# Kernel tuning notes

Measured on AMD Instinct MI355X. Metric: run time of the kernel, lower is better.

## Reference

```python
import jax, jax.numpy as jnp
import numpy as np


def setup_inputs() -> dict:
    key = jax.random.key(0)
    k1, k2, k3, k4 = jax.random.split(key, 4)
    B, N, D_in, H, P = 16, 4096, 588, 1152, 4096
    pixel_values = jax.random.uniform(k1, (B, N, D_in), dtype=jnp.float32)
    pixel_position_ids = jax.random.randint(k2, (B, N, 2), 0, P, dtype=jnp.int64)
    padding_positions = jnp.zeros((B, N), dtype=bool)
    W_proj = jax.random.normal(k3, (D_in, H), dtype=jnp.float32) * (D_in ** -0.5)
    pos_table = jax.random.normal(k4, (2, P, H), dtype=jnp.float32)
    return {
        "pixel_values": pixel_values,
        "pixel_position_ids": pixel_position_ids,
        "padding_positions": padding_positions,
        "W_proj": W_proj,
        "pos_table": pos_table,
    }


def reference(pixel_values, pixel_position_ids, padding_positions, W_proj, pos_table):
    # Patch projection: patches = 2*(x - 0.5); Linear(no bias).
    patches = 2.0 * (pixel_values - 0.5)
    hidden = jnp.einsum("bnd,dh->bnh", patches, W_proj)  # [B,N,H]

    # Position embeddings: one_hot @ table summed over the 2 (row/col) axis
    # == gather of table rows. Same math, no [B,2,N,P] intermediate.
    pos = jnp.maximum(pixel_position_ids, 0)  # clamp(min=0), [B,N,2]
    pe = pos_table[0][pos[..., 0]] + pos_table[1][pos[..., 1]]  # [B,N,H]
    pe = jnp.where(padding_positions[..., None], 0.0, pe)

    return hidden + pe
```

## Files before the change

kernel.cpp:

```cpp
#include <hip/hip_runtime.h>
#include <hip/hip_bf16.h>
#include <stdint.h>

#define M_TOTAL   65536
#define K_ORIG    588
#define K_PAD     608
#define H_DIM     1152
#define P_DIM     4096
#define KT_STEPS  19

typedef short bf16x8 __attribute__((ext_vector_type(8)));
typedef float f32x4  __attribute__((ext_vector_type(4)));

__device__ __forceinline__ unsigned short f2bf(float f) {
  __hip_bfloat16 h = __float2bfloat16(f);
  return __builtin_bit_cast(unsigned short, h);
}

__device__ __forceinline__ void gload_lds16(const void* g, void* s) {
  __builtin_amdgcn_global_load_lds(
      (const __attribute__((address_space(1))) void*)g,
      (__attribute__((address_space(3))) void*)s, 16, 0, 0);
}

__global__ void convert_patches(const float* __restrict__ px,
                                unsigned short* __restrict__ out) {
  const int64_t i = (int64_t)blockIdx.x * blockDim.x + threadIdx.x;
  const int g = (int)(i % 152);
  const int64_t m = i / 152;
  const int k0 = g * 4;
  ushort4 o;
  if (k0 < K_ORIG) {
    const float4 v = *(const float4*)(px + m * K_ORIG + k0);
    o.x = f2bf(2.f * v.x - 1.f);
    o.y = f2bf(2.f * v.y - 1.f);
    o.z = f2bf(2.f * v.z - 1.f);
    o.w = f2bf(2.f * v.w - 1.f);
  } else {
    o.x = 0; o.y = 0; o.z = 0; o.w = 0;
  }
  *(ushort4*)(out + m * K_PAD + k0) = o;
}

__global__ void convert_w(const float* __restrict__ W,
                          unsigned short* __restrict__ Wt) {
  const int i = blockIdx.x * blockDim.x + threadIdx.x;
  const int k = i % K_PAD;
  const int h = i / K_PAD;
  Wt[i] = (k < K_ORIG) ? f2bf(W[(int64_t)k * H_DIM + h]) : (unsigned short)0;
}

__global__ void __launch_bounds__(256) gemm_fused(
    const unsigned short* __restrict__ A,
    const unsigned short* __restrict__ Bt,
    const int* __restrict__ ids,
    const unsigned char* __restrict__ padm,
    const float* __restrict__ ptab,
    float* __restrict__ out) {
  __shared__ __align__(16) unsigned short Ash[128 * 32];
  __shared__ __align__(16) unsigned short Bsh[128 * 32];
  __shared__ int p0s[128];
  __shared__ int p1s[128];
  __shared__ unsigned char mks[128];

  const int tid = threadIdx.x;
  const int w   = tid >> 6;
  const int l   = tid & 63;
  const int bm  = blockIdx.x / 9;
  const int bn  = blockIdx.x % 9;
  const int wm  = w >> 1;
  const int wn  = w & 1;

  if (tid < 128) {
    const int gm = bm * 128 + tid;
    const int q0 = ids[2 * gm + 0];
    const int q1 = ids[2 * gm + 1];
    p0s[tid] = q0 < 0 ? 0 : q0;
    p1s[tid] = q1 < 0 ? 0 : q1;
    mks[tid] = padm[gm];
  }

  f32x4 acc[4][4];
#pragma unroll
  for (int i = 0; i < 4; ++i)
#pragma unroll
    for (int j = 0; j < 4; ++j) acc[i][j] = f32x4{0.f, 0.f, 0.f, 0.f};

  const int srow = l >> 2;
  const int sk   = ((l & 3) ^ ((l >> 3) & 3)) * 8;
  const int64_t abase = (int64_t)(bm * 128) * K_PAD;
  const int64_t bbase = (int64_t)(bn * 128) * K_PAD;

  int ra[4], rb[4];
#pragma unroll
  for (int mi = 0; mi < 4; ++mi) {
    const int rA = wm * 64 + mi * 16 + (l & 15);
    ra[mi] = rA * 32 + (((l >> 4) ^ ((rA >> 1) & 3)) * 8);
    const int rB = wn * 64 + mi * 16 + (l & 15);
    rb[mi] = rB * 32 + (((l >> 4) ^ ((rB >> 1) & 3)) * 8);
  }

  for (int kt = 0; kt < KT_STEPS; ++kt) {
    const int k0 = kt * 32;
#pragma unroll
    for (int i = 0; i < 2; ++i) {
      const int r0 = (w * 2 + i) * 16;
      gload_lds16(A + abase + (int64_t)(r0 + srow) * K_PAD + k0 + sk,
                  &Ash[r0 * 32]);
      gload_lds16(Bt + bbase + (int64_t)(r0 + srow) * K_PAD + k0 + sk,
                  &Bsh[r0 * 32]);
    }
    __syncthreads();

    bf16x8 av[4], bv[4];
#pragma unroll
    for (int mi = 0; mi < 4; ++mi) av[mi] = *(const bf16x8*)&Ash[ra[mi]];
#pragma unroll
    for (int ni = 0; ni < 4; ++ni) bv[ni] = *(const bf16x8*)&Bsh[rb[ni]];
#pragma unroll
    for (int mi = 0; mi < 4; ++mi)
#pragma unroll
      for (int ni = 0; ni < 4; ++ni)
        acc[mi][ni] = __builtin_amdgcn_mfma_f32_16x16x32_bf16(
            av[mi], bv[ni], acc[mi][ni], 0, 0, 0);
    __syncthreads();
  }

  const int c  = l & 15;
  const int rg = (l >> 4) * 4;
  const float* T0 = ptab;
  const float* T1 = ptab + (int64_t)P_DIM * H_DIM;
  const int hcol0 = bn * 128 + wn * 64;

#pragma unroll
  for (int mi = 0; mi < 4; ++mi) {
#pragma unroll
    for (int j = 0; j < 4; ++j) {
      const int r = wm * 64 + mi * 16 + rg + j;
      const int64_t gm = (int64_t)bm * 128 + r;
      const bool pad = mks[r] != 0;
      const float* t0 = T0 + (int64_t)p0s[r] * H_DIM;
      const float* t1 = T1 + (int64_t)p1s[r] * H_DIM;
      float* orow = out + gm * H_DIM;
#pragma unroll
      for (int ni = 0; ni < 4; ++ni) {
        const int gh = hcol0 + ni * 16 + c;
        const float pe = pad ? 0.f : (t0[gh] + t1[gh]);
        orow[gh] = acc[mi][ni][j] + pe;
      }
    }
  }
}

extern "C" void kernel_launch(void* const* d_in, const int* in_sizes, int n_in,
                              void* d_out, int out_size, void* d_ws,
                              size_t ws_size, hipStream_t stream) {
  const float* px            = (const float*)d_in[0];
  const int* ids             = (const int*)d_in[1];
  const unsigned char* padm  = (const unsigned char*)d_in[2];
  const float* W             = (const float*)d_in[3];
  const float* pt            = (const float*)d_in[4];
  float* out                 = (float*)d_out;

  unsigned short* Apad = (unsigned short*)d_ws;
  unsigned short* Wt   = Apad + (size_t)M_TOTAL * K_PAD;

  convert_patches<<<38912, 256, 0, stream>>>(px, Apad);
  convert_w<<<2736, 256, 0, stream>>>(W, Wt);
  gemm_fused<<<4608, 256, 0, stream>>>(Apad, Wt, ids, padm, pt, out);
}
```

Baseline: 651.9 us.

## Fuse patch fp32-to-bf16 conversion into GEMM with double-buffered LDS pipeline

Drops the separate convert_patches pass. The GEMM now reads fp32 pixel values directly into registers, scales and converts them to bf16, and writes them into swizzled LDS. A double-buffered LDS scheme prefetches the next K-tile of A (through registers) and B (direct-to-LDS) while the current tile is computed, which halves the number of barriers. It also remaps block indices so that consecutive blocks spread across groups, and rewrites the weight transpose to use a shared-memory tile for coalesced access. The cost is that each of the 9 column blocks per row tile re-reads and re-converts the fp32 A tile, at twice the bytes of bf16, and register and LDS use go up.

```diff
diff --git a/kernel.cpp b/kernel.cpp
--- a/kernel.cpp
+++ b/kernel.cpp
@@ -23,42 +23,36 @@
       (__attribute__((address_space(3))) void*)s, 16, 0, 0);
 }
 
-__global__ void convert_patches(const float* __restrict__ px,
-                                unsigned short* __restrict__ out) {
-  const int64_t i = (int64_t)blockIdx.x * blockDim.x + threadIdx.x;
-  const int g = (int)(i % 152);
-  const int64_t m = i / 152;
-  const int k0 = g * 4;
-  ushort4 o;
-  if (k0 < K_ORIG) {
-    const float4 v = *(const float4*)(px + m * K_ORIG + k0);
-    o.x = f2bf(2.f * v.x - 1.f);
-    o.y = f2bf(2.f * v.y - 1.f);
-    o.z = f2bf(2.f * v.z - 1.f);
-    o.w = f2bf(2.f * v.w - 1.f);
-  } else {
-    o.x = 0; o.y = 0; o.z = 0; o.w = 0;
-  }
-  *(ushort4*)(out + m * K_PAD + k0) = o;
-}
-
-__global__ void convert_w(const float* __restrict__ W,
-                          unsigned short* __restrict__ Wt) {
-  const int i = blockIdx.x * blockDim.x + threadIdx.x;
-  const int k = i % K_PAD;
-  const int h = i / K_PAD;
-  Wt[i] = (k < K_ORIG) ? f2bf(W[(int64_t)k * H_DIM + h]) : (unsigned short)0;
+__global__ void __launch_bounds__(256) convert_w(const float* __restrict__ W,
+                                                 unsigned short* __restrict__ Wt) {
+  __shared__ float tile[32][33];
+  const int kt = blockIdx.x % 19;
+  const int ht = blockIdx.x / 19;
+  const int k0 = kt * 32, h0 = ht * 32;
+  const int r = threadIdx.x >> 5;
+  const int c = threadIdx.x & 31;
+#pragma unroll
+  for (int i = 0; i < 4; ++i) {
+    const int k = k0 + r + i * 8;
+    tile[r + i * 8][c] = (k < K_ORIG) ? W[(int64_t)k * H_DIM + h0 + c] : 0.f;
+  }
+  __syncthreads();
+#pragma unroll
+  for (int i = 0; i < 4; ++i) {
+    const int h = h0 + r + i * 8;
+    Wt[(int64_t)h * K_PAD + k0 + c] = f2bf(tile[c][r + i * 8]);
+  }
 }
 
 __global__ void __launch_bounds__(256) gemm_fused(
-    const unsigned short* __restrict__ A,
+    const float* __restrict__ px,
     const unsigned short* __restrict__ Bt,
     const int* __restrict__ ids,
     const unsigned char* __restrict__ padm,
     const float* __restrict__ ptab,
     float* __restrict__ out) {
-  __shared__ __align__(16) unsigned short Ash[128 * 32];
-  __shared__ __align__(16) unsigned short Bsh[128 * 32];
+  __shared__ __align__(16) unsigned short Ash[2][128 * 32];
+  __shared__ __align__(16) unsigned short Bsh[2][128 * 32];
   __shared__ int p0s[128];
   __shared__ int p1s[128];
   __shared__ unsigned char mks[128];
@@ -66,8 +60,11 @@
   const int tid = threadIdx.x;
   const int w   = tid >> 6;
   const int l   = tid & 63;
-  const int bm  = blockIdx.x / 9;
-  const int bn  = blockIdx.x % 9;
+
+  const int bid = blockIdx.x;
+  const int lin = (bid >> 3) + (bid & 7) * 576;
+  const int bm  = lin / 9;
+  const int bn  = lin % 9;
   const int wm  = w >> 1;
   const int wn  = w & 1;
 
@@ -88,8 +85,12 @@
 
   const int srow = l >> 2;
   const int sk   = ((l & 3) ^ ((l >> 3) & 3)) * 8;
-  const int64_t abase = (int64_t)(bm * 128) * K_PAD;
   const int64_t bbase = (int64_t)(bn * 128) * K_PAD;
+
+  const int arow = tid >> 3;
+  const int achk = tid & 7;
+  const int64_t arowbase = (int64_t)(bm * 128) * K_ORIG;
+  f32x4 areg[4];
 
   int ra[4], rb[4];
 #pragma unroll
@@ -100,30 +101,73 @@
     rb[mi] = rB * 32 + (((l >> 4) ^ ((rB >> 1) & 3)) * 8);
   }
 
-  for (int kt = 0; kt < KT_STEPS; ++kt) {
+  auto stageB = [&](int kt, int buf) {
     const int k0 = kt * 32;
 #pragma unroll
     for (int i = 0; i < 2; ++i) {
       const int r0 = (w * 2 + i) * 16;
-      gload_lds16(A + abase + (int64_t)(r0 + srow) * K_PAD + k0 + sk,
-                  &Ash[r0 * 32]);
       gload_lds16(Bt + bbase + (int64_t)(r0 + srow) * K_PAD + k0 + sk,
-                  &Bsh[r0 * 32]);
-    }
-    __syncthreads();
+                  &Bsh[buf][r0 * 32]);
+    }
+  };
+
+  auto loadA = [&](int kt) {
+    const int k = kt * 32 + achk * 4;
+    const bool v = (k < K_ORIG);
+    const f32x4 zero = {0.f, 0.f, 0.f, 0.f};
+#pragma unroll
+    for (int rb4 = 0; rb4 < 4; ++rb4) {
+      const int row = rb4 * 32 + arow;
+      areg[rb4] = v ? *(const f32x4*)(px + arowbase + (int64_t)row * K_ORIG + k)
+                    : zero;
+    }
+  };
+
+  auto writeA = [&](int buf) {
+    const int g   = achk >> 1;
+    const int sub = (achk & 1) * 4;
+#pragma unroll
+    for (int rb4 = 0; rb4 < 4; ++rb4) {
+      const int row = rb4 * 32 + arow;
+      const int off = row * 32 + ((g ^ ((row >> 1) & 3)) * 8) + sub;
+      ushort4 o;
+      o.x = f2bf(__builtin_fmaf(2.f, areg[rb4][0], -1.f));
+      o.y = f2bf(__builtin_fmaf(2.f, areg[rb4][1], -1.f));
+      o.z = f2bf(__builtin_fmaf(2.f, areg[rb4][2], -1.f));
+      o.w = f2bf(__builtin_fmaf(2.f, areg[rb4][3], -1.f));
+      *(ushort4*)&Ash[buf][off] = o;
+    }
+  };
+
+  loadA(0);
+  stageB(0, 0);
+  writeA(0);
+  __syncthreads();
+
+  for (int t = 0; t < KT_STEPS; ++t) {
+    const int cur = t & 1;
+    const bool more = (t + 1 < KT_STEPS);
+    if (more) {
+      stageB(t + 1, cur ^ 1);
+      loadA(t + 1);
+    }
 
     bf16x8 av[4], bv[4];
 #pragma unroll
-    for (int mi = 0; mi < 4; ++mi) av[mi] = *(const bf16x8*)&Ash[ra[mi]];
-#pragma unroll
-    for (int ni = 0; ni < 4; ++ni) bv[ni] = *(const bf16x8*)&Bsh[rb[ni]];
+    for (int mi = 0; mi < 4; ++mi) av[mi] = *(const bf16x8*)&Ash[cur][ra[mi]];
+#pragma unroll
+    for (int ni = 0; ni < 4; ++ni) bv[ni] = *(const bf16x8*)&Bsh[cur][rb[ni]];
 #pragma unroll
     for (int mi = 0; mi < 4; ++mi)
 #pragma unroll
       for (int ni = 0; ni < 4; ++ni)
         acc[mi][ni] = __builtin_amdgcn_mfma_f32_16x16x32_bf16(
             av[mi], bv[ni], acc[mi][ni], 0, 0, 0);
-    __syncthreads();
+
+    if (more) {
+      writeA(cur ^ 1);
+      __syncthreads();
+    }
   }
 
   const int c  = l & 15;
@@ -162,10 +206,8 @@
   const float* pt            = (const float*)d_in[4];
   float* out                 = (float*)d_out;
 
-  unsigned short* Apad = (unsigned short*)d_ws;
-  unsigned short* Wt   = Apad + (size_t)M_TOTAL * K_PAD;
-
-  convert_patches<<<38912, 256, 0, stream>>>(px, Apad);
-  convert_w<<<2736, 256, 0, stream>>>(W, Wt);
-  gemm_fused<<<4608, 256, 0, stream>>>(Apad, Wt, ids, padm, pt, out);
-}
+  unsigned short* Wt = (unsigned short*)d_ws;
+
+  convert_w<<<19 * 36, 256, 0, stream>>>(W, Wt);
+  gemm_fused<<<4608, 256, 0, stream>>>(px, Wt, ids, padm, pt, out);
+}
```

Result: faster. 638.5 us (-2.0%).
